# Performance work log

Measured on AMD Instinct MI355X. Metric: run time of the kernel, lower is better.

The kernel has to match this reference:

```python
import jax, jax.numpy as jnp
import numpy as np

E = 250000   # n_scanned_edges
B = 16       # batch_size
N = 50000    # n_entities (n_nodes)
R = 500      # n_relations
D_IN = 100   # input embedding dim (proj input)
D = 64       # n_dims_sm
M = 2 * E    # n_memorized_and_scanned_nodes (>= n_vi_groups + n_vj_groups)


def setup_inputs() -> dict:
    rng = np.random.default_rng(0)
    eg = rng.integers(0, B, E)
    vi = rng.integers(0, N, E)
    vj = rng.integers(0, N, E)
    order = np.lexsort((vj, vi, eg))  # sorted by (eg_idx, vi, vj) as the module assumes
    eg, vi, vj = eg[order], vi[order], vj[order]
    rel = rng.integers(0, R, E)
    # dense group ids; idx_vi is non-decreasing because edges are lexsorted by (eg,vi)
    idx_vi = np.unique(eg.astype(np.int64) * N + vi, return_inverse=True)[1]
    idx_vj = np.unique(eg.astype(np.int64) * N + vj, return_inverse=True)[1]
    n_vi = int(idx_vi.max()) + 1
    edges = np.stack([eg, vi, vj, rel, idx_vi, idx_vj, idx_vi, n_vi + idx_vj], 1).astype(np.int32)

    key = jax.random.key(0)
    ks = jax.random.split(key, 24)
    nrm = lambda k, shp, s=1.0: jax.random.normal(k, shp, jnp.float32) * s
    na = jax.random.uniform(ks[0], (B, N), jnp.float32)
    na = na / jnp.sum(na, 1, keepdims=True)  # node attention is a distribution per example
    inp = {
        "node_attention": na,
        "scanned_edges": jnp.asarray(edges),
        "hidden_uncon": nrm(ks[1], (1, N, D_IN)),
        "hidden_con": nrm(ks[2], (M, D_IN)),
        "rel_table": nrm(ks[3], (R, D_IN)),
        "query_head_emb": nrm(ks[4], (B, D_IN)),
        "query_rel_emb": nrm(ks[5], (B, D_IN)),
        "p_W": nrm(ks[6], (D_IN, D), 0.1),
        "p_b": jnp.zeros((D,), jnp.float32),
    }
    i = 7
    for g in ("g1", "g2"):
        for nm, shp in (("lW", (4 * D, D)), ("lb", (D,)), ("rW", (4 * D, D)), ("rb", (D,)), ("cW", (D, D)), ("cb", (D,))):
            inp[g + "_" + nm] = nrm(ks[i], shp, 0.05)
            i += 1
    return inp


def _g(left, right, lW, lb, rW, rb, cW, cb):
    # G layer: sum(left_dense(cat(left)) * center_dense(right_dense(cat(right))), -1)
    lx = jnp.concatenate(left, -1)
    rx = jnp.concatenate(right, -1)
    l = jax.nn.leaky_relu(lx @ lW + lb, 0.2)  # tf.nn.leaky_relu alpha=0.2
    r = jax.nn.leaky_relu(rx @ rW + rb, 0.2)
    return jnp.sum(l * (r @ cW + cb), -1)


def reference(node_attention, scanned_edges, hidden_uncon, hidden_con, rel_table,
              query_head_emb, query_rel_emb, p_W, p_b,
              g1_lW, g1_lb, g1_rW, g1_rb, g1_cW, g1_cb,
              g2_lW, g2_lb, g2_rW, g2_rb, g2_cW, g2_cb):
    Bn, Nn = node_attention.shape
    En = scanned_edges.shape[0]
    proj = lambda x: jnp.tanh(x @ p_W + p_b)

    h_con = proj(hidden_con)       # (M, D)
    h_uncon = proj(hidden_uncon)   # (1, N, D)
    qh = proj(query_head_emb)      # (B, D)
    qr = proj(query_rel_emb)

    e = scanned_edges
    eg, vi, vj = e[:, 0], e[:, 1], e[:, 2]
    idx_vi = e[:, 4]
    # node2edge gathers
    h_vi = h_con[e[:, 6]]          # (E, D)
    h_vj = h_con[e[:, 7]]
    hu_vj = h_uncon[0][vj]         # hidden_uncon batch is 1 -> idx 0
    remb = proj(rel_table[e[:, 3]])
    qhv = qh[eg]
    qrv = qr[eg]

    left = (h_vi, remb, qhv, qrv)
    logits = _g(left, (h_vj, remb, qhv, qrv), g1_lW, g1_lb, g1_rW, g1_rb, g1_cW, g1_cb)
    logits = logits + _g(left, (hu_vj, remb, qhv, qrv), g2_lW, g2_lb, g2_rW, g2_rb, g2_cW, g2_cb)

    # neighbor softmax over sorted idx_vi segments
    m = jax.ops.segment_max(logits, idx_vi, num_segments=En, indices_are_sorted=True)
    ex = jnp.exp(logits - m[idx_vi])
    den = jax.ops.segment_sum(ex, idx_vi, num_segments=En, indices_are_sorted=True)
    transition = ex / den[idx_vi]

    # flow attention: gather at (eg, vi), scatter-sum at (eg, vj)
    trans_att = node_attention[eg, vi] * transition
    new_att = jnp.zeros((Bn, Nn), node_attention.dtype).at[eg, vj].add(trans_att)
    new_att = new_att / jnp.sum(new_att, axis=1, keepdims=True)
    return new_att
```

## Files before the change

kernel.cpp:

```cpp
#include <hip/hip_runtime.h>

#define DIN 100
#define DD  64
#define NE  250000
#define NB  16
#define NN  50000
#define NR  500
#define NM  500000
#define NH  (NM + NN)

#define H_OFF    64
#define TA2_OFF  (H_OFF + NH*DD)
#define RT_OFF   (TA2_OFF + NE*DD)
#define QT_OFF   (RT_OFF + 4*NR*DD)
#define LG_OFF   (QT_OFF + 4*NB*DD)

#define PA 320
#define PB 160
#define PC 32

#define XT_STRIDE 260

#define PROJ_LDSF (64*104)

__device__ __forceinline__ void fma4x4(const float4 x, const float4 w, float4 acc[4]) {
  acc[0].x += x.x*w.x; acc[0].y += x.x*w.y; acc[0].z += x.x*w.z; acc[0].w += x.x*w.w;
  acc[1].x += x.y*w.x; acc[1].y += x.y*w.y; acc[1].z += x.y*w.z; acc[1].w += x.y*w.w;
  acc[2].x += x.z*w.x; acc[2].y += x.z*w.y; acc[2].z += x.z*w.z; acc[2].w += x.z*w.w;
  acc[3].x += x.w*w.x; acc[3].y += x.w*w.y; acc[3].z += x.w*w.z; acc[3].w += x.w*w.w;
}

__device__ __forceinline__ float4 leaky4(float4 v) {
  v.x = v.x > 0.f ? v.x : 0.2f*v.x;
  v.y = v.y > 0.f ? v.y : 0.2f*v.y;
  v.z = v.z > 0.f ? v.z : 0.2f*v.z;
  v.w = v.w > 0.f ? v.w : 0.2f*v.w;
  return v;
}

__global__ void k_init(int* wsI, float* bsum) {
  if (threadIdx.x == 0) { wsI[0] = 0x7fffffff; wsI[1] = 0; }
  if (threadIdx.x < NB) bsum[threadIdx.x] = 0.f;
}

__global__ void k_limits(const int* __restrict__ edges, int* __restrict__ wsI) {
  int i = blockIdx.x * blockDim.x + threadIdx.x;
  int mn = 0x7fffffff, mx = -1;
  if (i < NE) { int v = edges[i*8 + 7]; mn = v; mx = v; }
  for (int off = 32; off > 0; off >>= 1) {
    mn = min(mn, __shfl_down(mn, off));
    mx = max(mx, __shfl_down(mx, off));
  }
  if ((threadIdx.x & 63) == 0) {
    atomicMin(&wsI[0], mn);
    atomicMax(&wsI[1], mx + 1);
  }
}

__global__ void k_tables(const float* __restrict__ rtab,
                         const float* __restrict__ qh, const float* __restrict__ qr,
                         const float* __restrict__ pW, const float* __restrict__ pb,
                         const float* __restrict__ g1_lW, const float* __restrict__ g1_lb,
                         const float* __restrict__ g1_rW, const float* __restrict__ g1_rb,
                         const float* __restrict__ g2_lW, const float* __restrict__ g2_lb,
                         const float* __restrict__ g2_rW, const float* __restrict__ g2_rb,
                         float* __restrict__ rT, float* __restrict__ qT) {
  __shared__ float xs[DIN], xs2[DIN], ps[DD], ps2[DD];
  const int d = threadIdx.x;
  const int blk = blockIdx.x;
  if (blk < NR) {
    for (int k = d; k < DIN; k += 64) xs[k] = rtab[blk*DIN + k];
    __syncthreads();
    float a = pb[d];
    for (int k = 0; k < DIN; ++k) a += xs[k] * pW[k*DD + d];
    ps[d] = tanhf(a);
    __syncthreads();
    float o1 = 0.f, o2 = 0.f, o3 = 0.f, o4 = 0.f;
    for (int k = 0; k < DD; ++k) {
      float p = ps[k];
      o1 += p * g1_lW[(DD + k)*DD + d];
      o2 += p * g1_rW[(DD + k)*DD + d];
      o3 += p * g2_lW[(DD + k)*DD + d];
      o4 += p * g2_rW[(DD + k)*DD + d];
    }
    rT[(0*NR + blk)*DD + d] = o1;
    rT[(1*NR + blk)*DD + d] = o2;
    rT[(2*NR + blk)*DD + d] = o3;
    rT[(3*NR + blk)*DD + d] = o4;
  } else {
    const int b = blk - NR;
    for (int k = d; k < DIN; k += 64) { xs[k] = qh[b*DIN + k]; xs2[k] = qr[b*DIN + k]; }
    __syncthreads();
    float a = pb[d], a2 = pb[d];
    for (int k = 0; k < DIN; ++k) { a += xs[k]*pW[k*DD + d]; a2 += xs2[k]*pW[k*DD + d]; }
    ps[d] = tanhf(a); ps2[d] = tanhf(a2);
    __syncthreads();
    float o1 = g1_lb[d], o2 = g1_rb[d], o3 = g2_lb[d], o4 = g2_rb[d];
    for (int k = 0; k < DD; ++k) {
      float p = ps[k], p2 = ps2[k];
      o1 += p * g1_lW[(2*DD + k)*DD + d] + p2 * g1_lW[(3*DD + k)*DD + d];
      o2 += p * g1_rW[(2*DD + k)*DD + d] + p2 * g1_rW[(3*DD + k)*DD + d];
      o3 += p * g2_lW[(2*DD + k)*DD + d] + p2 * g2_lW[(3*DD + k)*DD + d];
      o4 += p * g2_rW[(2*DD + k)*DD + d] + p2 * g2_rW[(3*DD + k)*DD + d];
    }
    qT[(0*NB + b)*DD + d] = o1;
    qT[(1*NB + b)*DD + d] = o2;
    qT[(2*NB + b)*DD + d] = o3;
    qT[(3*NB + b)*DD + d] = o4;
  }
}

__global__ __launch_bounds__(256, 2)
void k_proj(const float* __restrict__ hcon, const float* __restrict__ huncon,
            const float* __restrict__ pW, const float* __restrict__ pb,
            const int* __restrict__ lim, float* __restrict__ H) {
  __shared__ __align__(16) float pWs[DIN*DD];
  __shared__ __align__(16) float Xb[2][PROJ_LDSF];
  const int tid  = threadIdx.x;
  for (int i = tid; i < DIN*DD; i += 256) pWs[i] = pW[i];
  const int lane = tid & 63, wid = tid >> 6;
  const int tc = tid & 15, tr = tid >> 4;
  const int c0 = tc << 2, r0 = tr << 2;
  const float4 pbv = *(const float4*)&pb[c0];
  const int nmax = lim[1];
  const int tA = (nmax + 63) >> 6;
  const int tB = (NN + 63) >> 6;
  const int NT = tA + tB;
  const int key = tr & 7;

#define STAGE_TILE(T, BUF)                                                      \
  {                                                                             \
    const float* sbase; int rbase, rlim;                                        \
    if ((T) < tA) { sbase = hcon;   rbase = (T) << 6;        rlim = NM; }       \
    else          { sbase = huncon; rbase = ((T) - tA) << 6; rlim = NN; }       \
    _Pragma("unroll")                                                           \
    for (int j = 0; j < 7; ++j) {                                               \
      int ii = j*4 + wid;                                                       \
      if (ii < 26) {                                                            \
        int p16  = ii*64 + lane;                                                \
        int row  = p16 / 26;                                                    \
        int slot = p16 - row*26;                                                \
        int kk4  = (slot < 24) ? (slot ^ ((row >> 2) & 7)) : 24;                \
        int grow = rbase + row; if (grow >= rlim) grow = rlim - 1;              \
        const float* gp = sbase + (size_t)grow*DIN + kk4*4;                     \
        __builtin_amdgcn_global_load_lds(                                       \
            (const __attribute__((address_space(1))) void*)gp,                  \
            (__attribute__((address_space(3))) void*)(&Xb[(BUF)][0] + ii*256),  \
            16, 0, 0);                                                          \
      }                                                                         \
    }                                                                           \
  }

  {
    int t0 = blockIdx.x;
    if (t0 < NT) STAGE_TILE(t0, 0);
  }
  __syncthreads();

  int it = 0;
  for (int t = blockIdx.x; t < NT; t += gridDim.x, ++it) {
    const int buf = it & 1;
    const int tn = t + gridDim.x;
    if (tn < NT) STAGE_TILE(tn, buf ^ 1);

    float4 acc[4];
    #pragma unroll
    for (int i = 0; i < 4; ++i) acc[i] = make_float4(0.f, 0.f, 0.f, 0.f);

    const float* Xp = &Xb[buf][0];
    for (int k4 = 0; k4 < 25; ++k4) {
      const int slot = (k4 < 24) ? (k4 ^ key) : 24;
      float4 xa0 = *(const float4*)&Xp[(r0 + 0)*104 + slot*4];
      float4 xa1 = *(const float4*)&Xp[(r0 + 1)*104 + slot*4];
      float4 xa2 = *(const float4*)&Xp[(r0 + 2)*104 + slot*4];
      float4 xa3 = *(const float4*)&Xp[(r0 + 3)*104 + slot*4];
      const float* wb = &pWs[k4*4*DD + c0];
      {
        float4 w = *(const float4*)&wb[0*DD];
        fma4x4(make_float4(xa0.x, xa1.x, xa2.x, xa3.x), w, acc);
      }
      {
        float4 w = *(const float4*)&wb[1*DD];
        fma4x4(make_float4(xa0.y, xa1.y, xa2.y, xa3.y), w, acc);
      }
      {
        float4 w = *(const float4*)&wb[2*DD];
        fma4x4(make_float4(xa0.z, xa1.z, xa2.z, xa3.z), w, acc);
      }
      {
        float4 w = *(const float4*)&wb[3*DD];
        fma4x4(make_float4(xa0.w, xa1.w, xa2.w, xa3.w), w, acc);
      }
    }

    const int row0 = (t < tA) ? (t << 6) : (NM + ((t - tA) << 6));
    #pragma unroll
    for (int i = 0; i < 4; ++i) {
      int row = row0 + r0 + i;
      if (row < NH) {
        float4 o;
        o.x = tanhf(acc[i].x + pbv.x);
        o.y = tanhf(acc[i].y + pbv.y);
        o.z = tanhf(acc[i].z + pbv.z);
        o.w = tanhf(acc[i].w + pbv.w);
        *(float4*)&H[(size_t)row*DD + c0] = o;
      }
    }
    __syncthreads();
  }
#undef STAGE_TILE
}

__global__ __launch_bounds__(256, 2)
void k_tf(const float* __restrict__ g1_lW, const float* __restrict__ g1_rW,
          const float* __restrict__ g2_lW, const float* __restrict__ g2_rW,
          const int* __restrict__ lim,
          float* __restrict__ H, float* __restrict__ TA2) {
  __shared__ __align__(16) float Ws0[DD*DD];
  __shared__ __align__(16) float Ws1[DD*DD];
  __shared__ __align__(16) float Ht[32][XT_STRIDE];
  const int tid = threadIdx.x;
  const int nvi  = lim[0];
  const int nmax = lim[1];
  int pool, pbase, pgrid;
  if (blockIdx.x < PA)           { pool = 0; pbase = blockIdx.x;           pgrid = PA; }
  else if (blockIdx.x < PA + PB) { pool = 1; pbase = blockIdx.x - PA;      pgrid = PB; }
  else                           { pool = 2; pbase = blockIdx.x - PA - PB; pgrid = PC; }
  if (pool == 0) {
    for (int i = tid; i < DD*DD; i += 256) { Ws0[i] = g1_lW[i]; Ws1[i] = g2_lW[i]; }
  } else if (pool == 1) {
    for (int i = tid; i < DD*DD; i += 256) Ws0[i] = g1_rW[i];
  } else {
    for (int i = tid; i < DD*DD; i += 256) Ws0[i] = g2_rW[i];
  }
  int t_begin, t_count, row_base;
  if (pool == 0)      { t_begin = 0;        t_count = (nvi + 255) >> 8;                 row_base = 0;  }
  else if (pool == 1) { t_begin = nvi >> 8; t_count = ((nmax + 255) >> 8) - (nvi >> 8); row_base = 0;  }
  else                { t_begin = 0;        t_count = (NN + 255) >> 8;                  row_base = NM; }
  const int tc = tid & 7, tr = tid >> 3;
  const int c0 = tc << 3;
  __syncthreads();
  for (int tt = pbase; tt < t_count; tt += pgrid) {
    const int row0 = row_base + ((t_begin + tt) << 8);
    const int myrow = row0 + tid;
    float4 a0[2][2][4], a1[2][2][4];
    #pragma unroll
    for (int a = 0; a < 2; ++a)
      #pragma unroll
      for (int b = 0; b < 2; ++b)
        #pragma unroll
        for (int i = 0; i < 4; ++i) {
          a0[a][b][i] = make_float4(0.f,0.f,0.f,0.f);
          a1[a][b][i] = make_float4(0.f,0.f,0.f,0.f);
        }
    #pragma unroll
    for (int chunk = 0; chunk < 2; ++chunk) {
      const int kb = chunk << 5;
      __syncthreads();
      if (myrow < NH) {
        const float* src = &H[(size_t)myrow*DD + kb];
        #pragma unroll
        for (int j = 0; j < 32; j += 4) {
          float4 v = *(const float4*)&src[j];
          Ht[j+0][tid] = v.x; Ht[j+1][tid] = v.y; Ht[j+2][tid] = v.z; Ht[j+3][tid] = v.w;
        }
      }
      __syncthreads();
      if (pool == 0) {
        for (int k = 0; k < 32; ++k) {
          float4 x0 = *(const float4*)&Ht[k][tr*8];
          float4 x1 = *(const float4*)&Ht[k][tr*8 + 4];
          float4 w0 = *(const float4*)&Ws0[(kb + k)*DD + c0];
          float4 w1 = *(const float4*)&Ws0[(kb + k)*DD + c0 + 4];
          float4 u0 = *(const float4*)&Ws1[(kb + k)*DD + c0];
          float4 u1 = *(const float4*)&Ws1[(kb + k)*DD + c0 + 4];
          fma4x4(x0, w0, a0[0][0]); fma4x4(x0, w1, a0[0][1]);
          fma4x4(x1, w0, a0[1][0]); fma4x4(x1, w1, a0[1][1]);
          fma4x4(x0, u0, a1[0][0]); fma4x4(x0, u1, a1[0][1]);
          fma4x4(x1, u0, a1[1][0]); fma4x4(x1, u1, a1[1][1]);
        }
      } else {
        for (int k = 0; k < 32; ++k) {
          float4 x0 = *(const float4*)&Ht[k][tr*8];
          float4 x1 = *(const float4*)&Ht[k][tr*8 + 4];
          float4 w0 = *(const float4*)&Ws0[(kb + k)*DD + c0];
          float4 w1 = *(const float4*)&Ws0[(kb + k)*DD + c0 + 4];
          fma4x4(x0, w0, a0[0][0]); fma4x4(x0, w1, a0[0][1]);
          fma4x4(x1, w0, a0[1][0]); fma4x4(x1, w1, a0[1][1]);
        }
      }
    }
    #pragma unroll
    for (int a = 0; a < 2; ++a)
      #pragma unroll
      for (int i = 0; i < 4; ++i) {
        int row = row0 + tr*8 + a*4 + i;
        bool ok;
        if (pool == 0)      ok = (row < nvi);
        else if (pool == 1) ok = (row >= nvi && row < nmax);
        else                ok = (row < NH);
        if (ok) {
          *(float4*)&H[row*DD + c0]     = a0[a][0][i];
          *(float4*)&H[row*DD + c0 + 4] = a0[a][1][i];
          if (pool == 0) {
            *(float4*)&TA2[row*DD + c0]     = a1[a][0][i];
            *(float4*)&TA2[row*DD + c0 + 4] = a1[a][1][i];
          }
        }
      }
  }
}

__global__ __launch_bounds__(256, 2)
void k_edges(const int* __restrict__ edges,
             const float* __restrict__ TA, const float* __restrict__ TA2,
             const float* __restrict__ HU2,
             const float* __restrict__ rT, const float* __restrict__ qT,
             const float* __restrict__ cW1, const float* __restrict__ cb1,
             const float* __restrict__ cW2, const float* __restrict__ cb2,
             float* __restrict__ logits) {
  __shared__ __align__(16) float Lt[DD][68];
  __shared__ __align__(16) float Rt[DD][68];
  __shared__ __align__(16) float4 cbs4[2][16];
  __shared__ float lg[64];
  __shared__ int   se[64*8];
  const int tid = threadIdx.x;
  if (tid < 16) {
    cbs4[0][tid] = *(const float4*)&cb1[tid*4];
    cbs4[1][tid] = *(const float4*)&cb2[tid*4];
  }
  const int e   = tid >> 2;
  const int d0  = (tid & 3) * 16;
  const int ee0 = (tid & 15) << 2;
  const int b0  = (tid >> 4) << 2;
  __syncthreads();
  const int NT = (NE + 63) / 64;
  for (int tile = blockIdx.x; tile < NT; tile += gridDim.x) {
    const int e0 = tile * 64;
    const int ecnt = min(64, NE - e0);
    for (int i = tid; i < 64*8; i += 256) se[i] = (i < ecnt*8) ? edges[e0*8 + i] : 0;
    if (tid < 64) lg[tid] = 0.f;
    __syncthreads();
    const int rel = se[e*8 + 3];
    const int eg  = se[e*8 + 0];
    const int li  = se[e*8 + 6];
    for (int g = 0; g < 2; ++g) {
      const float* Lb = g ? TA2 : TA;
      const float* Rb = g ? HU2 : TA;
      const float* rL = rT + (g ? 2*NR*DD : 0);
      const float* rR = rT + (g ? 3*NR*DD : 1*NR*DD);
      const float* qL = qT + (g ? 2*NB*DD : 0);
      const float* qR = qT + (g ? 3*NB*DD : 1*NB*DD);
      const float* cWg = g ? cW2 : cW1;
      const int ri = g ? se[e*8 + 2] : se[e*8 + 7];
      float cbp = 0.f;
      #pragma unroll
      for (int di = 0; di < 4; ++di) {
        const int d = d0 + 4*di;
        float4 l = *(const float4*)&Lb[li*DD + d];
        float4 t = *(const float4*)&rL[rel*DD + d];
        float4 u = *(const float4*)&qL[eg*DD + d];
        l.x += t.x + u.x; l.y += t.y + u.y; l.z += t.z + u.z; l.w += t.w + u.w;
        l = leaky4(l);
        Lt[d+0][e] = l.x; Lt[d+1][e] = l.y; Lt[d+2][e] = l.z; Lt[d+3][e] = l.w;
        float4 c = cbs4[g][d >> 2];
        cbp += l.x*c.x + l.y*c.y + l.z*c.z + l.w*c.w;
        float4 r = *(const float4*)&Rb[ri*DD + d];
        t = *(const float4*)&rR[rel*DD + d];
        u = *(const float4*)&qR[eg*DD + d];
        r.x += t.x + u.x; r.y += t.y + u.y; r.z += t.z + u.z; r.w += t.w + u.w;
        r = leaky4(r);
        Rt[d+0][e] = r.x; Rt[d+1][e] = r.y; Rt[d+2][e] = r.z; Rt[d+3][e] = r.w;
      }
      atomicAdd(&lg[e], cbp);
      __syncthreads();
      float4 z[4] = {{0,0,0,0},{0,0,0,0},{0,0,0,0},{0,0,0,0}};
      #pragma unroll 8
      for (int a = 0; a < DD; ++a) {
        float4 x = *(const float4*)&Rt[a][ee0];
        float4 w = *(const float4*)&cWg[a*DD + b0];
        fma4x4(x, w, z);
      }
      {
        float4 l0v = *(const float4*)&Lt[b0+0][ee0];
        float4 l1v = *(const float4*)&Lt[b0+1][ee0];
        float4 l2v = *(const float4*)&Lt[b0+2][ee0];
        float4 l3v = *(const float4*)&Lt[b0+3][ee0];
        float p0 = z[0].x*l0v.x + z[0].y*l1v.x + z[0].z*l2v.x + z[0].w*l3v.x;
        float p1 = z[1].x*l0v.y + z[1].y*l1v.y + z[1].z*l2v.y + z[1].w*l3v.y;
        float p2 = z[2].x*l0v.z + z[2].y*l1v.z + z[2].z*l2v.z + z[2].w*l3v.z;
        float p3 = z[3].x*l0v.w + z[3].y*l1v.w + z[3].z*l2v.w + z[3].w*l3v.w;
        atomicAdd(&lg[ee0+0], p0);
        atomicAdd(&lg[ee0+1], p1);
        atomicAdd(&lg[ee0+2], p2);
        atomicAdd(&lg[ee0+3], p3);
      }
      __syncthreads();
    }
    if (tid < ecnt) logits[e0 + tid] = lg[tid];
    __syncthreads();
  }
}

__global__ void k_softmax(const int* __restrict__ edges, const float* __restrict__ logits,
                          const float* __restrict__ na, float* __restrict__ out) {
  int e = blockIdx.x * blockDim.x + threadIdx.x;
  if (e >= NE) return;
  int seg = edges[e*8 + 4];
  if (e > 0 && edges[(e-1)*8 + 4] == seg) return;
  int j = e;
  float m = -1e30f;
  while (j < NE && edges[j*8 + 4] == seg) { m = fmaxf(m, logits[j]); ++j; }
  float s = 0.f;
  for (int t = e; t < j; ++t) s += expf(logits[t] - m);
  int eg = edges[e*8 + 0], vi = edges[e*8 + 1];
  float scale = na[eg*NN + vi] / s;
  for (int t = e; t < j; ++t) {
    int vj = edges[t*8 + 2];
    __hip_atomic_fetch_add(&out[eg*NN + vj], expf(logits[t] - m) * scale,
                           __ATOMIC_RELAXED, __HIP_MEMORY_SCOPE_AGENT);
  }
}

__global__ void k_rowsum(const float* __restrict__ out, float* __restrict__ bsum) {
  int b = blockIdx.y;
  float s = 0.f;
  for (int n = blockIdx.x * blockDim.x + threadIdx.x; n < NN; n += gridDim.x * blockDim.x)
    s += out[b*NN + n];
  for (int off = 32; off > 0; off >>= 1) s += __shfl_down(s, off);
  if ((threadIdx.x & 63) == 0)
    __hip_atomic_fetch_add(&bsum[b], s, __ATOMIC_RELAXED, __HIP_MEMORY_SCOPE_AGENT);
}

__global__ void k_div(float* __restrict__ out, const float* __restrict__ bsum) {
  int i = blockIdx.x * blockDim.x + threadIdx.x;
  if (i < NB*NN) out[i] /= bsum[i / NN];
}

extern "C" void kernel_launch(void* const* d_in, const int* in_sizes, int n_in,
                              void* d_out, int out_size, void* d_ws, size_t ws_size,
                              hipStream_t stream) {
  (void)in_sizes; (void)n_in; (void)out_size; (void)ws_size;
  const float* na     = (const float*)d_in[0];
  const int*   edges  = (const int*)  d_in[1];
  const float* huncon = (const float*)d_in[2];
  const float* hcon   = (const float*)d_in[3];
  const float* rtab   = (const float*)d_in[4];
  const float* qh     = (const float*)d_in[5];
  const float* qr     = (const float*)d_in[6];
  const float* pW     = (const float*)d_in[7];
  const float* pb     = (const float*)d_in[8];
  const float* g1_lW  = (const float*)d_in[9];
  const float* g1_lb  = (const float*)d_in[10];
  const float* g1_rW  = (const float*)d_in[11];
  const float* g1_rb  = (const float*)d_in[12];
  const float* g1_cW  = (const float*)d_in[13];
  const float* g1_cb  = (const float*)d_in[14];
  const float* g2_lW  = (const float*)d_in[15];
  const float* g2_lb  = (const float*)d_in[16];
  const float* g2_rW  = (const float*)d_in[17];
  const float* g2_rb  = (const float*)d_in[18];
  const float* g2_cW  = (const float*)d_in[19];
  const float* g2_cb  = (const float*)d_in[20];
  float* out  = (float*)d_out;
  float* ws   = (float*)d_ws;
  int*   wsI  = (int*)d_ws;
  float* bsum = ws + 16;
  float* H    = ws + H_OFF;
  float* TA2  = ws + TA2_OFF;
  float* rT   = ws + RT_OFF;
  float* qT   = ws + QT_OFF;
  float* lgp  = ws + LG_OFF;

  hipMemsetAsync(d_out, 0, (size_t)NB*NN*sizeof(float), stream);
  k_init<<<1, 64, 0, stream>>>(wsI, bsum);
  k_limits<<<(NE + 255)/256, 256, 0, stream>>>(edges, wsI);
  k_tables<<<NR + NB, 64, 0, stream>>>(rtab, qh, qr, pW, pb,
                                       g1_lW, g1_lb, g1_rW, g1_rb,
                                       g2_lW, g2_lb, g2_rW, g2_rb, rT, qT);
  k_proj<<<768, 256, 0, stream>>>(hcon, huncon, pW, pb, wsI, H);
  k_tf<<<PA + PB + PC, 256, 0, stream>>>(g1_lW, g1_rW, g2_lW, g2_rW, wsI, H, TA2);
  k_edges<<<1024, 256, 0, stream>>>(edges, H, TA2, H + NM*DD, rT, qT,
                                    g1_cW, g1_cb, g2_cW, g2_cb, lgp);
  k_softmax<<<(NE + 255)/256, 256, 0, stream>>>(edges, lgp, na, out);
  k_rowsum<<<dim3(32, 16), 256, 0, stream>>>(out, bsum);
  k_div<<<(NB*NN + 255)/256, 256, 0, stream>>>(out, bsum);
}
```

Before: 796.4 us.

## Restructure edge logits kernel into per-wavefront 16-edge tiles without block barriers

The edge kernel now gives each 64-lane wavefront its own tile of 16 edges, with private LDS slices. This removes every __syncthreads and all shared-memory atomicAdds. Each lane computes a 16-wide slice of the center dense product for one edge, and partial dot products are reduced with wave shuffles. The cost is more global/L1 traffic for cW, since each lane reads its own 16-column slice instead of sharing through a block tile. Correctness also relies on wavefront lockstep for the LDS write-then-read with no explicit barrier.

```diff
diff --git a/kernel.cpp b/kernel.cpp
--- a/kernel.cpp
+++ b/kernel.cpp
@@ -319,86 +319,95 @@
              const float* __restrict__ cW1, const float* __restrict__ cb1,
              const float* __restrict__ cW2, const float* __restrict__ cb2,
              float* __restrict__ logits) {
-  __shared__ __align__(16) float Lt[DD][68];
-  __shared__ __align__(16) float Rt[DD][68];
-  __shared__ __align__(16) float4 cbs4[2][16];
-  __shared__ float lg[64];
-  __shared__ int   se[64*8];
-  const int tid = threadIdx.x;
-  if (tid < 16) {
-    cbs4[0][tid] = *(const float4*)&cb1[tid*4];
-    cbs4[1][tid] = *(const float4*)&cb2[tid*4];
-  }
-  const int e   = tid >> 2;
-  const int d0  = (tid & 3) * 16;
-  const int ee0 = (tid & 15) << 2;
-  const int b0  = (tid >> 4) << 2;
-  __syncthreads();
-  const int NT = (NE + 63) / 64;
-  for (int tile = blockIdx.x; tile < NT; tile += gridDim.x) {
-    const int e0 = tile * 64;
-    const int ecnt = min(64, NE - e0);
-    for (int i = tid; i < 64*8; i += 256) se[i] = (i < ecnt*8) ? edges[e0*8 + i] : 0;
-    if (tid < 64) lg[tid] = 0.f;
-    __syncthreads();
-    const int rel = se[e*8 + 3];
-    const int eg  = se[e*8 + 0];
-    const int li  = se[e*8 + 6];
+  __shared__ __align__(16) float Lt[4][16][68];
+  __shared__ __align__(16) float Rt[4][16][68];
+  __shared__ int se[4][128];
+  const int tid  = threadIdx.x;
+  const int w    = tid >> 6, lane = tid & 63;
+  const int je   = lane & 15;
+  const int q    = lane >> 4;
+  const int d0   = q << 4;
+  float (*Ltw)[68] = Lt[w];
+  float (*Rtw)[68] = Rt[w];
+  int* sew = se[w];
+  const int NWT = (NE + 15) >> 4;
+  const int nw  = gridDim.x << 2;
+  for (int wt = (blockIdx.x << 2) + w; wt < NWT; wt += nw) {
+    const int e0   = wt << 4;
+    const int ecnt = min(16, NE - e0);
+    {
+      int i0 = lane;
+      sew[i0] = (i0 < ecnt*8) ? edges[e0*8 + i0] : 0;
+      int i1 = 64 + lane;
+      sew[i1] = (i1 < ecnt*8) ? edges[e0*8 + i1] : 0;
+    }
+    const int rel = sew[je*8 + 3];
+    const int eg  = sew[je*8 + 0];
+    const int li  = sew[je*8 + 6];
+    float plog = 0.f;
+    #pragma unroll 1
     for (int g = 0; g < 2; ++g) {
-      const float* Lb = g ? TA2 : TA;
-      const float* Rb = g ? HU2 : TA;
-      const float* rL = rT + (g ? 2*NR*DD : 0);
-      const float* rR = rT + (g ? 3*NR*DD : 1*NR*DD);
-      const float* qL = qT + (g ? 2*NB*DD : 0);
-      const float* qR = qT + (g ? 3*NB*DD : 1*NB*DD);
+      const float* Lb  = g ? TA2 : TA;
+      const float* Rb  = g ? HU2 : TA;
+      const float* rL  = rT + (g ? 2*NR*DD : 0);
+      const float* rR  = rT + (g ? 3*NR*DD : 1*NR*DD);
+      const float* qL  = qT + (g ? 2*NB*DD : 0);
+      const float* qR  = qT + (g ? 3*NB*DD : 1*NB*DD);
       const float* cWg = g ? cW2 : cW1;
-      const int ri = g ? se[e*8 + 2] : se[e*8 + 7];
+      const float* cbg = g ? cb2 : cb1;
+      const int    ri  = g ? sew[je*8 + 2] : sew[je*8 + 7];
       float cbp = 0.f;
       #pragma unroll
-      for (int di = 0; di < 4; ++di) {
-        const int d = d0 + 4*di;
-        float4 l = *(const float4*)&Lb[li*DD + d];
+      for (int j = 0; j < 4; ++j) {
+        const int d = d0 + 4*j;
+        float4 l = *(const float4*)&Lb[(size_t)li*DD + d];
         float4 t = *(const float4*)&rL[rel*DD + d];
         float4 u = *(const float4*)&qL[eg*DD + d];
         l.x += t.x + u.x; l.y += t.y + u.y; l.z += t.z + u.z; l.w += t.w + u.w;
         l = leaky4(l);
-        Lt[d+0][e] = l.x; Lt[d+1][e] = l.y; Lt[d+2][e] = l.z; Lt[d+3][e] = l.w;
-        float4 c = cbs4[g][d >> 2];
+        *(float4*)&Ltw[je][d] = l;
+        float4 c = *(const float4*)&cbg[d];
         cbp += l.x*c.x + l.y*c.y + l.z*c.z + l.w*c.w;
-        float4 r = *(const float4*)&Rb[ri*DD + d];
+        float4 r = *(const float4*)&Rb[(size_t)ri*DD + d];
         t = *(const float4*)&rR[rel*DD + d];
         u = *(const float4*)&qR[eg*DD + d];
         r.x += t.x + u.x; r.y += t.y + u.y; r.z += t.z + u.z; r.w += t.w + u.w;
         r = leaky4(r);
-        Rt[d+0][e] = r.x; Rt[d+1][e] = r.y; Rt[d+2][e] = r.z; Rt[d+3][e] = r.w;
-      }
-      atomicAdd(&lg[e], cbp);
-      __syncthreads();
-      float4 z[4] = {{0,0,0,0},{0,0,0,0},{0,0,0,0},{0,0,0,0}};
-      #pragma unroll 8
-      for (int a = 0; a < DD; ++a) {
-        float4 x = *(const float4*)&Rt[a][ee0];
-        float4 w = *(const float4*)&cWg[a*DD + b0];
-        fma4x4(x, w, z);
-      }
-      {
-        float4 l0v = *(const float4*)&Lt[b0+0][ee0];
-        float4 l1v = *(const float4*)&Lt[b0+1][ee0];
-        float4 l2v = *(const float4*)&Lt[b0+2][ee0];
-        float4 l3v = *(const float4*)&Lt[b0+3][ee0];
-        float p0 = z[0].x*l0v.x + z[0].y*l1v.x + z[0].z*l2v.x + z[0].w*l3v.x;
-        float p1 = z[1].x*l0v.y + z[1].y*l1v.y + z[1].z*l2v.y + z[1].w*l3v.y;
-        float p2 = z[2].x*l0v.z + z[2].y*l1v.z + z[2].z*l2v.z + z[2].w*l3v.z;
-        float p3 = z[3].x*l0v.w + z[3].y*l1v.w + z[3].z*l2v.w + z[3].w*l3v.w;
-        atomicAdd(&lg[ee0+0], p0);
-        atomicAdd(&lg[ee0+1], p1);
-        atomicAdd(&lg[ee0+2], p2);
-        atomicAdd(&lg[ee0+3], p3);
-      }
-      __syncthreads();
-    }
-    if (tid < ecnt) logits[e0 + tid] = lg[tid];
-    __syncthreads();
+        *(float4*)&Rtw[je][d] = r;
+      }
+      float4 z0 = make_float4(0,0,0,0), z1 = z0, z2 = z0, z3 = z0;
+      #pragma unroll 2
+      for (int ab = 0; ab < 16; ++ab) {
+        const int a = ab << 2;
+        float4 ra = *(const float4*)&Rtw[je][a];
+        #pragma unroll
+        for (int t = 0; t < 4; ++t) {
+          const float  r  = (t == 0) ? ra.x : (t == 1) ? ra.y : (t == 2) ? ra.z : ra.w;
+          const float* wr = &cWg[(a + t)*DD + d0];
+          float4 w0 = *(const float4*)&wr[0];
+          float4 w1 = *(const float4*)&wr[4];
+          float4 w2 = *(const float4*)&wr[8];
+          float4 w3 = *(const float4*)&wr[12];
+          z0.x += r*w0.x; z0.y += r*w0.y; z0.z += r*w0.z; z0.w += r*w0.w;
+          z1.x += r*w1.x; z1.y += r*w1.y; z1.z += r*w1.z; z1.w += r*w1.w;
+          z2.x += r*w2.x; z2.y += r*w2.y; z2.z += r*w2.z; z2.w += r*w2.w;
+          z3.x += r*w3.x; z3.y += r*w3.y; z3.z += r*w3.z; z3.w += r*w3.w;
+        }
+      }
+      float4 l0 = *(const float4*)&Ltw[je][d0 + 0];
+      float4 l1 = *(const float4*)&Ltw[je][d0 + 4];
+      float4 l2 = *(const float4*)&Ltw[je][d0 + 8];
+      float4 l3 = *(const float4*)&Ltw[je][d0 + 12];
+      float p = cbp
+              + z0.x*l0.x + z0.y*l0.y + z0.z*l0.z + z0.w*l0.w
+              + z1.x*l1.x + z1.y*l1.y + z1.z*l1.z + z1.w*l1.w
+              + z2.x*l2.x + z2.y*l2.y + z2.z*l2.z + z2.w*l2.w
+              + z3.x*l3.x + z3.y*l3.y + z3.z*l3.z + z3.w*l3.w;
+      p += __shfl_down(p, 32);
+      p += __shfl_down(p, 16);
+      plog += p;
+    }
+    if (lane < ecnt) logits[e0 + lane] = plog;
   }
 }
 
```

New measurement: 938.6 us. +17.9%, slower.

## Fuse projection and G-layer first-stage transforms into one kernel keeping tiles in LDS

Applied to the files above, without the earlier changes.

Merges the projection kernel and the transform kernel so that each 64-row tile is projected with tanh, staged in shared memory, and immediately multiplied by the relevant G-layer weights before writing H and TA2. This removes the round trip of the intermediate projected rows through global memory and one kernel launch. In exchange, the double-buffered async staging of input tiles is dropped, so loads no longer overlap compute. The transform weights are also now read from global memory instead of shared memory. Index arithmetic in the edge kernel is widened to size_t.

```diff
diff --git a/kernel.cpp b/kernel.cpp
--- a/kernel.cpp
+++ b/kernel.cpp
@@ -14,12 +14,6 @@
 #define RT_OFF   (TA2_OFF + NE*DD)
 #define QT_OFF   (RT_OFF + 4*NR*DD)
 #define LG_OFF   (QT_OFF + 4*NB*DD)
-
-#define PA 320
-#define PB 160
-#define PC 32
-
-#define XT_STRIDE 260
 
 #define PROJ_LDSF (64*104)
 
@@ -111,203 +105,162 @@
 }
 
 __global__ __launch_bounds__(256, 2)
-void k_proj(const float* __restrict__ hcon, const float* __restrict__ huncon,
-            const float* __restrict__ pW, const float* __restrict__ pb,
-            const int* __restrict__ lim, float* __restrict__ H) {
+void k_projtf(const float* __restrict__ hcon, const float* __restrict__ huncon,
+              const float* __restrict__ pW, const float* __restrict__ pb,
+              const float* __restrict__ g1_lW, const float* __restrict__ g1_rW,
+              const float* __restrict__ g2_lW, const float* __restrict__ g2_rW,
+              const int* __restrict__ lim,
+              float* __restrict__ H, float* __restrict__ TA2) {
   __shared__ __align__(16) float pWs[DIN*DD];
-  __shared__ __align__(16) float Xb[2][PROJ_LDSF];
+  __shared__ __align__(16) float Xb[PROJ_LDSF];
+  __shared__ __align__(16) float Ht[64][68];
   const int tid  = threadIdx.x;
   for (int i = tid; i < DIN*DD; i += 256) pWs[i] = pW[i];
   const int lane = tid & 63, wid = tid >> 6;
   const int tc = tid & 15, tr = tid >> 4;
   const int c0 = tc << 2, r0 = tr << 2;
   const float4 pbv = *(const float4*)&pb[c0];
+  const int nvi  = lim[0];
   const int nmax = lim[1];
   const int tA = (nmax + 63) >> 6;
-  const int tB = (NN + 63) >> 6;
-  const int NT = tA + tB;
+  const int NT = tA + ((NN + 63) >> 6);
   const int key = tr & 7;
 
-#define STAGE_TILE(T, BUF)                                                      \
-  {                                                                             \
-    const float* sbase; int rbase, rlim;                                        \
-    if ((T) < tA) { sbase = hcon;   rbase = (T) << 6;        rlim = NM; }       \
-    else          { sbase = huncon; rbase = ((T) - tA) << 6; rlim = NN; }       \
-    _Pragma("unroll")                                                           \
-    for (int j = 0; j < 7; ++j) {                                               \
-      int ii = j*4 + wid;                                                       \
-      if (ii < 26) {                                                            \
-        int p16  = ii*64 + lane;                                                \
-        int row  = p16 / 26;                                                    \
-        int slot = p16 - row*26;                                                \
-        int kk4  = (slot < 24) ? (slot ^ ((row >> 2) & 7)) : 24;                \
-        int grow = rbase + row; if (grow >= rlim) grow = rlim - 1;              \
-        const float* gp = sbase + (size_t)grow*DIN + kk4*4;                     \
-        __builtin_amdgcn_global_load_lds(                                       \
-            (const __attribute__((address_space(1))) void*)gp,                  \
-            (__attribute__((address_space(3))) void*)(&Xb[(BUF)][0] + ii*256),  \
-            16, 0, 0);                                                          \
-      }                                                                         \
-    }                                                                           \
-  }
-
-  {
-    int t0 = blockIdx.x;
-    if (t0 < NT) STAGE_TILE(t0, 0);
-  }
-  __syncthreads();
-
-  int it = 0;
-  for (int t = blockIdx.x; t < NT; t += gridDim.x, ++it) {
-    const int buf = it & 1;
-    const int tn = t + gridDim.x;
-    if (tn < NT) STAGE_TILE(tn, buf ^ 1);
+  auto gemm1 = [&](const float* __restrict__ W, float4 a[4]) {
+    #pragma unroll
+    for (int i = 0; i < 4; ++i) a[i] = make_float4(0.f,0.f,0.f,0.f);
+    for (int k4 = 0; k4 < 16; ++k4) {
+      float4 x0 = *(const float4*)&Ht[r0+0][k4*4];
+      float4 x1 = *(const float4*)&Ht[r0+1][k4*4];
+      float4 x2 = *(const float4*)&Ht[r0+2][k4*4];
+      float4 x3 = *(const float4*)&Ht[r0+3][k4*4];
+      const float* wb = &W[(k4*4)*DD + c0];
+      fma4x4(make_float4(x0.x,x1.x,x2.x,x3.x), *(const float4*)&wb[0],    a);
+      fma4x4(make_float4(x0.y,x1.y,x2.y,x3.y), *(const float4*)&wb[DD],   a);
+      fma4x4(make_float4(x0.z,x1.z,x2.z,x3.z), *(const float4*)&wb[2*DD], a);
+      fma4x4(make_float4(x0.w,x1.w,x2.w,x3.w), *(const float4*)&wb[3*DD], a);
+    }
+  };
+  auto gemm2 = [&](const float* __restrict__ W1, const float* __restrict__ W2,
+                   float4 a[4], float4 b[4]) {
+    #pragma unroll
+    for (int i = 0; i < 4; ++i) { a[i] = make_float4(0.f,0.f,0.f,0.f); b[i] = a[i]; }
+    for (int k4 = 0; k4 < 16; ++k4) {
+      float4 x0 = *(const float4*)&Ht[r0+0][k4*4];
+      float4 x1 = *(const float4*)&Ht[r0+1][k4*4];
+      float4 x2 = *(const float4*)&Ht[r0+2][k4*4];
+      float4 x3 = *(const float4*)&Ht[r0+3][k4*4];
+      float4 vx = make_float4(x0.x,x1.x,x2.x,x3.x);
+      float4 vy = make_float4(x0.y,x1.y,x2.y,x3.y);
+      float4 vz = make_float4(x0.z,x1.z,x2.z,x3.z);
+      float4 vw = make_float4(x0.w,x1.w,x2.w,x3.w);
+      const float* w1 = &W1[(k4*4)*DD + c0];
+      const float* w2 = &W2[(k4*4)*DD + c0];
+      fma4x4(vx, *(const float4*)&w1[0],    a);
+      fma4x4(vy, *(const float4*)&w1[DD],   a);
+      fma4x4(vz, *(const float4*)&w1[2*DD], a);
+      fma4x4(vw, *(const float4*)&w1[3*DD], a);
+      fma4x4(vx, *(const float4*)&w2[0],    b);
+      fma4x4(vy, *(const float4*)&w2[DD],   b);
+      fma4x4(vz, *(const float4*)&w2[2*DD], b);
+      fma4x4(vw, *(const float4*)&w2[3*DD], b);
+    }
+  };
+
+  for (int t = blockIdx.x; t < NT; t += gridDim.x) {
+    {
+      const float* sbase; int rbase, rlim;
+      if (t < tA) { sbase = hcon;   rbase = t << 6;        rlim = NM; }
+      else        { sbase = huncon; rbase = (t - tA) << 6; rlim = NN; }
+      #pragma unroll
+      for (int j = 0; j < 7; ++j) {
+        int ii = j*4 + wid;
+        if (ii < 26) {
+          int p16  = ii*64 + lane;
+          int row  = p16 / 26;
+          int slot = p16 - row*26;
+          int kk4  = (slot < 24) ? (slot ^ ((row >> 2) & 7)) : 24;
+          int grow = rbase + row; if (grow >= rlim) grow = rlim - 1;
+          const float* gp = sbase + (size_t)grow*DIN + kk4*4;
+          __builtin_amdgcn_global_load_lds(
+              (const __attribute__((address_space(1))) void*)gp,
+              (__attribute__((address_space(3))) void*)(&Xb[0] + ii*256),
+              16, 0, 0);
+        }
+      }
+    }
+    __syncthreads();
 
     float4 acc[4];
     #pragma unroll
     for (int i = 0; i < 4; ++i) acc[i] = make_float4(0.f, 0.f, 0.f, 0.f);
-
-    const float* Xp = &Xb[buf][0];
     for (int k4 = 0; k4 < 25; ++k4) {
       const int slot = (k4 < 24) ? (k4 ^ key) : 24;
-      float4 xa0 = *(const float4*)&Xp[(r0 + 0)*104 + slot*4];
-      float4 xa1 = *(const float4*)&Xp[(r0 + 1)*104 + slot*4];
-      float4 xa2 = *(const float4*)&Xp[(r0 + 2)*104 + slot*4];
-      float4 xa3 = *(const float4*)&Xp[(r0 + 3)*104 + slot*4];
+      float4 xa0 = *(const float4*)&Xb[(r0 + 0)*104 + slot*4];
+      float4 xa1 = *(const float4*)&Xb[(r0 + 1)*104 + slot*4];
+      float4 xa2 = *(const float4*)&Xb[(r0 + 2)*104 + slot*4];
+      float4 xa3 = *(const float4*)&Xb[(r0 + 3)*104 + slot*4];
       const float* wb = &pWs[k4*4*DD + c0];
-      {
-        float4 w = *(const float4*)&wb[0*DD];
-        fma4x4(make_float4(xa0.x, xa1.x, xa2.x, xa3.x), w, acc);
-      }
-      {
-        float4 w = *(const float4*)&wb[1*DD];
-        fma4x4(make_float4(xa0.y, xa1.y, xa2.y, xa3.y), w, acc);
-      }
-      {
-        float4 w = *(const float4*)&wb[2*DD];
-        fma4x4(make_float4(xa0.z, xa1.z, xa2.z, xa3.z), w, acc);
-      }
-      {
-        float4 w = *(const float4*)&wb[3*DD];
-        fma4x4(make_float4(xa0.w, xa1.w, xa2.w, xa3.w), w, acc);
-      }
-    }
-
-    const int row0 = (t < tA) ? (t << 6) : (NM + ((t - tA) << 6));
+      fma4x4(make_float4(xa0.x, xa1.x, xa2.x, xa3.x), *(const float4*)&wb[0],    acc);
+      fma4x4(make_float4(xa0.y, xa1.y, xa2.y, xa3.y), *(const float4*)&wb[DD],   acc);
+      fma4x4(make_float4(xa0.z, xa1.z, xa2.z, xa3.z), *(const float4*)&wb[2*DD], acc);
+      fma4x4(make_float4(xa0.w, xa1.w, xa2.w, xa3.w), *(const float4*)&wb[3*DD], acc);
+    }
     #pragma unroll
     for (int i = 0; i < 4; ++i) {
-      int row = row0 + r0 + i;
-      if (row < NH) {
-        float4 o;
-        o.x = tanhf(acc[i].x + pbv.x);
-        o.y = tanhf(acc[i].y + pbv.y);
-        o.z = tanhf(acc[i].z + pbv.z);
-        o.w = tanhf(acc[i].w + pbv.w);
-        *(float4*)&H[(size_t)row*DD + c0] = o;
-      }
-    }
-    __syncthreads();
-  }
-#undef STAGE_TILE
-}
-
-__global__ __launch_bounds__(256, 2)
-void k_tf(const float* __restrict__ g1_lW, const float* __restrict__ g1_rW,
-          const float* __restrict__ g2_lW, const float* __restrict__ g2_rW,
-          const int* __restrict__ lim,
-          float* __restrict__ H, float* __restrict__ TA2) {
-  __shared__ __align__(16) float Ws0[DD*DD];
-  __shared__ __align__(16) float Ws1[DD*DD];
-  __shared__ __align__(16) float Ht[32][XT_STRIDE];
-  const int tid = threadIdx.x;
-  const int nvi  = lim[0];
-  const int nmax = lim[1];
-  int pool, pbase, pgrid;
-  if (blockIdx.x < PA)           { pool = 0; pbase = blockIdx.x;           pgrid = PA; }
-  else if (blockIdx.x < PA + PB) { pool = 1; pbase = blockIdx.x - PA;      pgrid = PB; }
-  else                           { pool = 2; pbase = blockIdx.x - PA - PB; pgrid = PC; }
-  if (pool == 0) {
-    for (int i = tid; i < DD*DD; i += 256) { Ws0[i] = g1_lW[i]; Ws1[i] = g2_lW[i]; }
-  } else if (pool == 1) {
-    for (int i = tid; i < DD*DD; i += 256) Ws0[i] = g1_rW[i];
-  } else {
-    for (int i = tid; i < DD*DD; i += 256) Ws0[i] = g2_rW[i];
-  }
-  int t_begin, t_count, row_base;
-  if (pool == 0)      { t_begin = 0;        t_count = (nvi + 255) >> 8;                 row_base = 0;  }
-  else if (pool == 1) { t_begin = nvi >> 8; t_count = ((nmax + 255) >> 8) - (nvi >> 8); row_base = 0;  }
-  else                { t_begin = 0;        t_count = (NN + 255) >> 8;                  row_base = NM; }
-  const int tc = tid & 7, tr = tid >> 3;
-  const int c0 = tc << 3;
-  __syncthreads();
-  for (int tt = pbase; tt < t_count; tt += pgrid) {
-    const int row0 = row_base + ((t_begin + tt) << 8);
-    const int myrow = row0 + tid;
-    float4 a0[2][2][4], a1[2][2][4];
-    #pragma unroll
-    for (int a = 0; a < 2; ++a)
-      #pragma unroll
-      for (int b = 0; b < 2; ++b)
-        #pragma unroll
-        for (int i = 0; i < 4; ++i) {
-          a0[a][b][i] = make_float4(0.f,0.f,0.f,0.f);
-          a1[a][b][i] = make_float4(0.f,0.f,0.f,0.f);
+      float4 o;
+      o.x = tanhf(acc[i].x + pbv.x);
+      o.y = tanhf(acc[i].y + pbv.y);
+      o.z = tanhf(acc[i].z + pbv.z);
+      o.w = tanhf(acc[i].w + pbv.w);
+      *(float4*)&Ht[r0 + i][c0] = o;
+    }
+    __syncthreads();
+
+    const int row0 = (t < tA) ? (t << 6) : (NM + ((t - tA) << 6));
+    if (t >= tA) {
+      float4 a1[4];
+      gemm1(g2_rW, a1);
+      #pragma unroll
+      for (int i = 0; i < 4; ++i) {
+        int row = row0 + r0 + i;
+        if (row < NH) *(float4*)&H[(size_t)row*DD + c0] = a1[i];
+      }
+    } else if (row0 + 64 <= nvi) {
+      float4 a1[4], a2[4];
+      gemm2(g1_lW, g2_lW, a1, a2);
+      #pragma unroll
+      for (int i = 0; i < 4; ++i) {
+        int row = row0 + r0 + i;
+        *(float4*)&H[(size_t)row*DD + c0]   = a1[i];
+        *(float4*)&TA2[(size_t)row*DD + c0] = a2[i];
+      }
+    } else if (row0 >= nvi) {
+      float4 a1[4];
+      gemm1(g1_rW, a1);
+      #pragma unroll
+      for (int i = 0; i < 4; ++i) {
+        int row = row0 + r0 + i;
+        if (row < nmax) *(float4*)&H[(size_t)row*DD + c0] = a1[i];
+      }
+    } else {
+      float4 a1[4], a2[4];
+      gemm2(g1_lW, g2_lW, a1, a2);
+      #pragma unroll
+      for (int i = 0; i < 4; ++i) {
+        int row = row0 + r0 + i;
+        if (row < nvi) {
+          *(float4*)&H[(size_t)row*DD + c0]   = a1[i];
+          *(float4*)&TA2[(size_t)row*DD + c0] = a2[i];
         }
-    #pragma unroll
-    for (int chunk = 0; chunk < 2; ++chunk) {
-      const int kb = chunk << 5;
-      __syncthreads();
-      if (myrow < NH) {
-        const float* src = &H[(size_t)myrow*DD + kb];
-        #pragma unroll
-        for (int j = 0; j < 32; j += 4) {
-          float4 v = *(const float4*)&src[j];
-          Ht[j+0][tid] = v.x; Ht[j+1][tid] = v.y; Ht[j+2][tid] = v.z; Ht[j+3][tid] = v.w;
-        }
-      }
-      __syncthreads();
-      if (pool == 0) {
-        for (int k = 0; k < 32; ++k) {
-          float4 x0 = *(const float4*)&Ht[k][tr*8];
-          float4 x1 = *(const float4*)&Ht[k][tr*8 + 4];
-          float4 w0 = *(const float4*)&Ws0[(kb + k)*DD + c0];
-          float4 w1 = *(const float4*)&Ws0[(kb + k)*DD + c0 + 4];
-          float4 u0 = *(const float4*)&Ws1[(kb + k)*DD + c0];
-          float4 u1 = *(const float4*)&Ws1[(kb + k)*DD + c0 + 4];
-          fma4x4(x0, w0, a0[0][0]); fma4x4(x0, w1, a0[0][1]);
-          fma4x4(x1, w0, a0[1][0]); fma4x4(x1, w1, a0[1][1]);
-          fma4x4(x0, u0, a1[0][0]); fma4x4(x0, u1, a1[0][1]);
-          fma4x4(x1, u0, a1[1][0]); fma4x4(x1, u1, a1[1][1]);
-        }
-      } else {
-        for (int k = 0; k < 32; ++k) {
-          float4 x0 = *(const float4*)&Ht[k][tr*8];
-          float4 x1 = *(const float4*)&Ht[k][tr*8 + 4];
-          float4 w0 = *(const float4*)&Ws0[(kb + k)*DD + c0];
-          float4 w1 = *(const float4*)&Ws0[(kb + k)*DD + c0 + 4];
-          fma4x4(x0, w0, a0[0][0]); fma4x4(x0, w1, a0[0][1]);
-          fma4x4(x1, w0, a0[1][0]); fma4x4(x1, w1, a0[1][1]);
-        }
-      }
-    }
-    #pragma unroll
-    for (int a = 0; a < 2; ++a)
+      }
+      gemm1(g1_rW, a1);
       #pragma unroll
       for (int i = 0; i < 4; ++i) {
-        int row = row0 + tr*8 + a*4 + i;
-        bool ok;
-        if (pool == 0)      ok = (row < nvi);
-        else if (pool == 1) ok = (row >= nvi && row < nmax);
-        else                ok = (row < NH);
-        if (ok) {
-          *(float4*)&H[row*DD + c0]     = a0[a][0][i];
-          *(float4*)&H[row*DD + c0 + 4] = a0[a][1][i];
-          if (pool == 0) {
-            *(float4*)&TA2[row*DD + c0]     = a1[a][0][i];
-            *(float4*)&TA2[row*DD + c0 + 4] = a1[a][1][i];
-          }
-        }
-      }
+        int row = row0 + r0 + i;
+        if (row >= nvi && row < nmax) *(float4*)&H[(size_t)row*DD + c0] = a1[i];
+      }
+    }
   }
 }
 
@@ -357,7 +310,7 @@
       #pragma unroll
       for (int di = 0; di < 4; ++di) {
         const int d = d0 + 4*di;
-        float4 l = *(const float4*)&Lb[li*DD + d];
+        float4 l = *(const float4*)&Lb[(size_t)li*DD + d];
         float4 t = *(const float4*)&rL[rel*DD + d];
         float4 u = *(const float4*)&qL[eg*DD + d];
         l.x += t.x + u.x; l.y += t.y + u.y; l.z += t.z + u.z; l.w += t.w + u.w;
@@ -365,7 +318,7 @@
         Lt[d+0][e] = l.x; Lt[d+1][e] = l.y; Lt[d+2][e] = l.z; Lt[d+3][e] = l.w;
         float4 c = cbs4[g][d >> 2];
         cbp += l.x*c.x + l.y*c.y + l.z*c.z + l.w*c.w;
-        float4 r = *(const float4*)&Rb[ri*DD + d];
+        float4 r = *(const float4*)&Rb[(size_t)ri*DD + d];
         t = *(const float4*)&rR[rel*DD + d];
         u = *(const float4*)&qR[eg*DD + d];
         r.x += t.x + u.x; r.y += t.y + u.y; r.z += t.z + u.z; r.w += t.w + u.w;
@@ -478,8 +431,8 @@
   k_tables<<<NR + NB, 64, 0, stream>>>(rtab, qh, qr, pW, pb,
                                        g1_lW, g1_lb, g1_rW, g1_rb,
                                        g2_lW, g2_lb, g2_rW, g2_rb, rT, qT);
-  k_proj<<<768, 256, 0, stream>>>(hcon, huncon, pW, pb, wsI, H);
-  k_tf<<<PA + PB + PC, 256, 0, stream>>>(g1_lW, g1_rW, g2_lW, g2_rW, wsI, H, TA2);
+  k_projtf<<<768, 256, 0, stream>>>(hcon, huncon, pW, pb,
+                                    g1_lW, g1_rW, g2_lW, g2_rW, wsI, H, TA2);
   k_edges<<<1024, 256, 0, stream>>>(edges, H, TA2, H + NM*DD, rT, qT,
                                     g1_cW, g1_cb, g2_cW, g2_cb, lgp);
   k_softmax<<<(NE + 255)/256, 256, 0, stream>>>(edges, lgp, na, out);
```

Measured after the change: 880.9 us. +10.6%, slower.
